# Optimization experiments

Hardware: AMD Instinct MI355X
Metric: run time of the kernel (lower is better)

## Reference

```python
import jax, jax.numpy as jnp
from jax import lax
import numpy as np

N_ASSETS = 256
BATCH = 512
MAX_WEIGHT = 0.05
N_ITERS = 300       # FISTA iterations (fixed, jit-friendly)
BISECT_ITERS = 60   # bisection iterations for the simplex-box projection
POWER_ITERS = 30    # power iterations for Lipschitz constant


def _project_capped_simplex(v, c):
    """Project rows of v onto {w : sum(w)=1, -c <= w <= c}.

    Finds tau s.t. sum(clip(v - tau, -c, c)) = 1 by bisection (non-diff),
    then recomputes tau exactly from the active-set mask so the projection
    is correctly differentiable (piecewise-linear Jacobian).
    """
    vs = lax.stop_gradient(v)
    lo = jnp.min(vs, axis=-1) - c   # sum = +n*c > 1 here
    hi = jnp.max(vs, axis=-1) + c   # sum = -n*c < 1 here

    def bis(carry, _):
        lo, hi = carry
        mid = 0.5 * (lo + hi)
        s = jnp.sum(jnp.clip(vs - mid[:, None], -c, c), axis=-1)
        lo = jnp.where(s > 1.0, mid, lo)
        hi = jnp.where(s > 1.0, hi, mid)
        return (lo, hi), None

    (lo, hi), _ = lax.scan(bis, (lo, hi), None, length=BISECT_ITERS)
    tau0 = 0.5 * (lo + hi)
    z = vs - tau0[:, None]
    interior = (jnp.abs(z) < c).astype(v.dtype)          # unclipped coords
    k_hi = jnp.sum((z >= c).astype(v.dtype), axis=-1)    # clipped at +c
    k_lo = jnp.sum((z <= -c).astype(v.dtype), axis=-1)   # clipped at -c
    denom = jnp.maximum(jnp.sum(interior, axis=-1), 1.0)
    # exact tau given the (stop-gradient) active set -> correct Jacobian in v
    tau = (jnp.sum(interior * v, axis=-1) + c * (k_hi - k_lo) - 1.0) / denom
    return jnp.clip(v - tau[:, None], -c, c)


def _min_var_weights(covmat_sqrt, c):
    """argmin_w ||A w||^2  s.t. sum(w)=1, -c<=w<=c  (batched FISTA)."""
    B, n, _ = covmat_sqrt.shape
    # Q = A^T A (the objective only depends on A through Q)
    Q = jnp.einsum('bij,bik->bjk', covmat_sqrt, covmat_sqrt)

    # power iteration for lambda_max(Q) -> step size 1/L, L = 2*lambda_max
    u = jnp.ones((B, n), covmat_sqrt.dtype) / jnp.sqrt(jnp.asarray(n, covmat_sqrt.dtype))

    def pit(u, _):
        u = jnp.einsum('bij,bj->bi', Q, u)
        u = u / (jnp.linalg.norm(u, axis=-1, keepdims=True) + 1e-12)
        return u, None

    u, _ = lax.scan(pit, u, None, length=POWER_ITERS)
    lmax = jnp.einsum('bi,bij,bj->b', u, Q, u)
    step = lax.stop_gradient(1.0 / (2.0 * lmax + 1e-12))[:, None]

    w0 = _project_capped_simplex(jnp.full((B, n), 1.0 / n, covmat_sqrt.dtype), c)

    @jax.checkpoint
    def fista(carry, _):
        w, y, t = carry
        g = 2.0 * jnp.einsum('bij,bj->bi', Q, y)
        w_new = _project_capped_simplex(y - step * g, c)
        t_new = 0.5 * (1.0 + jnp.sqrt(1.0 + 4.0 * t * t))
        y_new = w_new + ((t - 1.0) / t_new) * (w_new - w)
        return (w_new, y_new, t_new), None

    t0 = jnp.asarray(1.0, covmat_sqrt.dtype)
    (w, _, _), _ = lax.scan(fista, (w0, w0, t0), None, length=N_ITERS)
    return w


def setup_inputs() -> dict:
    key = jax.random.key(0)
    covmat_sqrt = jax.random.normal(
        key, (BATCH, N_ASSETS, N_ASSETS), dtype=jnp.float32
    ) / np.sqrt(N_ASSETS).astype(np.float32)
    return {"covmat_sqrt": covmat_sqrt}


def reference(covmat_sqrt):
    return _min_var_weights(covmat_sqrt, MAX_WEIGHT)
```

## Files before the change

kernel.cpp:

```cpp
#include <hip/hip_runtime.h>
#include <math.h>


#define NA    256
#define CAPW  0.05f

typedef float v2f __attribute__((ext_vector_type(2)));

template<int CTRL, int RM>
__device__ __forceinline__ float dpp0(float x) {
    return __int_as_float(__builtin_amdgcn_update_dpp(
        0, __float_as_int(x), CTRL, RM, 0xf, true));
}
template<int CTRL, int RM>
__device__ __forceinline__ float dppI(float x, float ident) {
    return __int_as_float(__builtin_amdgcn_update_dpp(
        __float_as_int(ident), __float_as_int(x), CTRL, RM, 0xf, false));
}
__device__ __forceinline__ float bcast63(float x) {
    return __int_as_float(__builtin_amdgcn_readlane(__float_as_int(x), 63));
}
__device__ __forceinline__ float wsum(float x) {
    x += dpp0<0x111, 0xf>(x);
    x += dpp0<0x112, 0xf>(x);
    x += dpp0<0x114, 0xf>(x);
    x += dpp0<0x118, 0xf>(x);
    x += dpp0<0x142, 0xa>(x);
    x += dpp0<0x143, 0xc>(x);
    return bcast63(x);
}
__device__ __forceinline__ float wmax(float x) {
    const float I = -1e30f;
    x = fmaxf(x, dppI<0x111, 0xf>(x, I));
    x = fmaxf(x, dppI<0x112, 0xf>(x, I));
    x = fmaxf(x, dppI<0x114, 0xf>(x, I));
    x = fmaxf(x, dppI<0x118, 0xf>(x, I));
    x = fmaxf(x, dppI<0x142, 0xa>(x, I));
    x = fmaxf(x, dppI<0x143, 0xc>(x, I));
    return bcast63(x);
}

__global__ void __launch_bounds__(512, 2)
markowitz_fista(const float* __restrict__ A, float* __restrict__ out)
{
    __shared__ float lds_pool[32 * 256];
    __shared__ int   done_flag;

    float* A_lds = lds_pool;
    float* p_lds = lds_pool;
    float* y_lds = lds_pool + 2048;

    const int tid = threadIdx.x;
    const int b   = blockIdx.x;
    const int r4  = tid & 63;
    const int e   = tid >> 6;
    const int R0  = r4 * 4;
    const int C0  = e * 32;

    const float* __restrict__ Ab = A + (size_t)b * NA * NA;

    v2f q2[4][16];
    #pragma unroll
    for (int a = 0; a < 4; ++a)
        #pragma unroll
        for (int k = 0; k < 16; ++k) q2[a][k] = (v2f){0.0f, 0.0f};

    for (int it = 0; it < 8; ++it) {
        __syncthreads();
        const float4* src = (const float4*)(Ab + it * 32 * 256);
        float4* dst = (float4*)A_lds;
        #pragma unroll
        for (int qd = 0; qd < 4; ++qd) dst[qd * 512 + tid] = src[qd * 512 + tid];
        __syncthreads();
        for (int ii = 0; ii < 32; ++ii) {
            const float* row = A_lds + ii * 256;
            float4 rv = *(const float4*)(row + R0);
            v2f r0 = {rv.x, rv.x}, r1 = {rv.y, rv.y}, r2 = {rv.z, rv.z}, r3 = {rv.w, rv.w};
            #pragma unroll
            for (int cc = 0; cc < 8; ++cc) {
                float4 cv = *(const float4*)(row + C0 + 4 * cc);
                v2f clo = {cv.x, cv.y}, chi = {cv.z, cv.w};
                q2[0][2*cc  ] = __builtin_elementwise_fma(r0, clo, q2[0][2*cc  ]);
                q2[0][2*cc+1] = __builtin_elementwise_fma(r0, chi, q2[0][2*cc+1]);
                q2[1][2*cc  ] = __builtin_elementwise_fma(r1, clo, q2[1][2*cc  ]);
                q2[1][2*cc+1] = __builtin_elementwise_fma(r1, chi, q2[1][2*cc+1]);
                q2[2][2*cc  ] = __builtin_elementwise_fma(r2, clo, q2[2][2*cc  ]);
                q2[2][2*cc+1] = __builtin_elementwise_fma(r2, chi, q2[2][2*cc+1]);
                q2[3][2*cc  ] = __builtin_elementwise_fma(r3, clo, q2[3][2*cc  ]);
                q2[3][2*cc+1] = __builtin_elementwise_fma(r3, chi, q2[3][2*cc+1]);
            }
        }
    }
    __syncthreads();

    auto partials = [&](bool chk) -> bool {
        __syncthreads();
        int fl = chk ? done_flag : 0;
        v2f aL0 = {0,0}, aL1 = {0,0}, aL2 = {0,0}, aL3 = {0,0};
        v2f aH0 = {0,0}, aH1 = {0,0}, aH2 = {0,0}, aH3 = {0,0};
        const float* yv = y_lds + C0;
        #pragma unroll
        for (int cc = 0; cc < 8; ++cc) {
            float4 y4 = *(const float4*)(yv + 4 * cc);
            v2f ylo = {y4.x, y4.y}, yhi = {y4.z, y4.w};
            aL0 = __builtin_elementwise_fma(q2[0][2*cc  ], ylo, aL0);
            aH0 = __builtin_elementwise_fma(q2[0][2*cc+1], yhi, aH0);
            aL1 = __builtin_elementwise_fma(q2[1][2*cc  ], ylo, aL1);
            aH1 = __builtin_elementwise_fma(q2[1][2*cc+1], yhi, aH1);
            aL2 = __builtin_elementwise_fma(q2[2][2*cc  ], ylo, aL2);
            aH2 = __builtin_elementwise_fma(q2[2][2*cc+1], yhi, aH2);
            aL3 = __builtin_elementwise_fma(q2[3][2*cc  ], ylo, aL3);
            aH3 = __builtin_elementwise_fma(q2[3][2*cc+1], yhi, aH3);
        }
        if (fl) return true;
        v2f s0 = aL0 + aH0, s1 = aL1 + aH1, s2 = aL2 + aH2, s3 = aL3 + aH3;
        *(float4*)(p_lds + e * 256 + R0) =
            make_float4(s0.x + s0.y, s1.x + s1.y, s2.x + s2.y, s3.x + s3.y);
        __syncthreads();
        return false;
    };
    auto reduceg = [&]() -> float4 {
        float4 r = *(const float4*)(p_lds + 4 * tid);
        #pragma unroll
        for (int ee = 1; ee < 8; ++ee) {
            float4 pv = *(const float4*)(p_lds + ee * 256 + 4 * tid);
            r.x += pv.x; r.y += pv.y; r.z += pv.z; r.w += pv.w;
        }
        return r;
    };

    if (tid < 64) {
        *(float4*)(y_lds + 4 * tid) = make_float4(0.0625f, 0.0625f, 0.0625f, 0.0625f);
    }
    float u0 = 0.0625f, u1 = 0.0625f, u2 = 0.0625f, u3 = 0.0625f;
    for (int p = 0; p < 30; ++p) {
        partials(false);
        if (tid < 64) {
            float4 g4 = reduceg();
            u0 = 0.25f * g4.x; u1 = 0.25f * g4.y;
            u2 = 0.25f * g4.z; u3 = 0.25f * g4.w;
            *(float4*)(y_lds + 4 * tid) = make_float4(u0, u1, u2, u3);
        }
    }
    partials(false);

    float step2 = 0.f, t = 1.0f, tau_ws = 0.0f, tau_pv = 0.0f, rm = 0.0f;
    float cnt_ws = 256.0f;
    float wa = 0.f, wb = 0.f, wc = 0.f, wd = 0.f;
    float ya = 0.f, yb = 0.f, yc = 0.f, yd = 0.f;
    if (tid < 64) {
        float4 g4 = reduceg();
        float num = wsum(u0*g4.x + u1*g4.y + u2*g4.z + u3*g4.w);
        float den = wsum(u0*u0 + u1*u1 + u2*u2 + u3*u3);
        float lm = num / (den + 1e-30f);
        float step = 1.0f / (2.0f * lm + 1e-12f);
        step2 = 2.0f * step;
        wa = wb = wc = wd = 1.0f / 256.0f;
        ya = yb = yc = yd = 1.0f / 256.0f;
        *(float4*)(y_lds + 4 * tid) = make_float4(ya, yb, yc, yd);
    }
    if (tid == 0) done_flag = 0;

    for (int itn = 0; itn < 300; ++itn) {
        if (partials(true)) break;
        if (tid < 64) {
            float4 g4 = reduceg();
            float v0 = ya - step2 * g4.x;
            float v1 = yb - step2 * g4.y;
            float v2 = yc - step2 * g4.z;
            float v3 = yd - step2 * g4.w;

            float lo = -2.0f, hi = 2.0f;
            float tau = fminf(fmaxf(tau_ws + (tau_ws - tau_pv), lo), hi);

            float s = 0.f, sm1 = 0.f;
            float tau_p = 0.f, s_p = 0.f;
            bool havep = false, have = false;
            for (int ni = 0; ni < 10; ++ni) {
                float z0 = v0 - tau, z1 = v1 - tau, z2 = v2 - tau, z3 = v3 - tau;
                float c0 = fminf(fmaxf(z0, -CAPW), CAPW);
                float c1 = fminf(fmaxf(z1, -CAPW), CAPW);
                float c2 = fminf(fmaxf(z2, -CAPW), CAPW);
                float c3 = fminf(fmaxf(z3, -CAPW), CAPW);
                s = wsum((c0 + c1) + (c2 + c3));
                sm1 = s - 1.0f;
                if (fabsf(sm1) <= 1e-4f) { have = true; break; }
                if (sm1 > 0.0f) lo = tau; else hi = tau;
                float m = fmaxf(cnt_ws, 1.0f);
                if (havep) {
                    float dt = tau - tau_p;
                    float ds = s_p - s;
                    float mm = ds / dt;
                    if (mm > 0.5f && mm == mm) m = mm;
                }
                float tn2 = tau + sm1 / m;
                if (!(tn2 > lo && tn2 < hi)) tn2 = 0.5f * (lo + hi);
                tau_p = tau; s_p = s; havep = true;
                tau = tn2;
            }
            if (!have) {
                float z0 = v0 - tau, z1 = v1 - tau, z2 = v2 - tau, z3 = v3 - tau;
                float c0 = fminf(fmaxf(z0, -CAPW), CAPW);
                float c1 = fminf(fmaxf(z1, -CAPW), CAPW);
                float c2 = fminf(fmaxf(z2, -CAPW), CAPW);
                float c3 = fminf(fmaxf(z3, -CAPW), CAPW);
                s = wsum((c0 + c1) + (c2 + c3));
                sm1 = s - 1.0f;
            }
            {
                float z0 = v0 - tau, z1 = v1 - tau, z2 = v2 - tau, z3 = v3 - tau;
                float cnt = wsum((fabsf(z0) < CAPW ? 1.f : 0.f) +
                                 (fabsf(z1) < CAPW ? 1.f : 0.f) +
                                 (fabsf(z2) < CAPW ? 1.f : 0.f) +
                                 (fabsf(z3) < CAPW ? 1.f : 0.f));
                cnt_ws = cnt;
                tau = tau + sm1 / fmaxf(cnt, 1.0f);
            }
            tau_pv = tau_ws;
            tau_ws = tau;
            float w0n = fminf(fmaxf(v0 - tau, -CAPW), CAPW);
            float w1n = fminf(fmaxf(v1 - tau, -CAPW), CAPW);
            float w2n = fminf(fmaxf(v2 - tau, -CAPW), CAPW);
            float w3n = fminf(fmaxf(v3 - tau, -CAPW), CAPW);

            float tn = 0.5f * (1.0f + sqrtf(1.0f + 4.0f * t * t));
            float beta = (t - 1.0f) / tn;
            float y0n = w0n + beta * (w0n - wa);
            float y1n = w1n + beta * (w1n - wb);
            float y2n = w2n + beta * (w2n - wc);
            float y3n = w3n + beta * (w3n - wd);

            *(float4*)(y_lds + 4 * tid) = make_float4(y0n, y1n, y2n, y3n);

            float dm = fmaxf(fmaxf(fabsf(w0n - wa), fabsf(w1n - wb)),
                             fmaxf(fabsf(w2n - wc), fabsf(w3n - wd)));
            rm = fmaxf(rm, dm);
            if ((itn & 7) == 7) {
                float rmax = wmax(rm);
                if (rmax < 1e-7f && tid == 0) done_flag = 1;
                rm = 0.0f;
            }

            wa = w0n; wb = w1n; wc = w2n; wd = w3n;
            ya = y0n; yb = y1n; yc = y2n; yd = y3n;
            t = tn;
        }
    }

    if (tid < 64) {
        *(float4*)(out + b * 256 + 4 * tid) = make_float4(wa, wb, wc, wd);
    }
}

extern "C" void kernel_launch(void* const* d_in, const int* in_sizes, int n_in,
                              void* d_out, int out_size, void* d_ws, size_t ws_size,
                              hipStream_t stream) {
    (void)in_sizes; (void)n_in; (void)d_ws; (void)ws_size; (void)out_size;
    const float* A = (const float*)d_in[0];
    float* out = (float*)d_out;
    hipLaunchKernelGGL(markowitz_fista, dim3(512), dim3(512), 0, stream, A, out);
}
```

Baseline: 933.9 us.

## Fold step into partials, precompute momentum on spare wave, speculate two tau guesses

The gradient step scale (-2*step) is stored in LDS and multiplied into the per-row partial products, so the wave doing the reduction only adds. FISTA momentum coefficients are computed one iteration ahead by a thread in the second wave and double-buffered in LDS, which takes the sqrt/divide off the critical serial wave. The projection now evaluates two candidate taus (the warm start and its extrapolation) together with their interior counts before entering a shorter Newton/bisection loop. This aims to cut serial latency per iteration on the single active wave, at the cost of extra wave reductions when neither guess converges.

```diff
diff --git a/kernel.cpp b/kernel.cpp
--- a/kernel.cpp
+++ b/kernel.cpp
@@ -96,6 +96,7 @@
     auto partials = [&](bool chk) -> bool {
         __syncthreads();
         int fl = chk ? done_flag : 0;
+        float scl = lds_pool[2304];
         v2f aL0 = {0,0}, aL1 = {0,0}, aL2 = {0,0}, aL3 = {0,0};
         v2f aH0 = {0,0}, aH1 = {0,0}, aH2 = {0,0}, aH3 = {0,0};
         const float* yv = y_lds + C0;
@@ -115,7 +116,8 @@
         if (fl) return true;
         v2f s0 = aL0 + aH0, s1 = aL1 + aH1, s2 = aL2 + aH2, s3 = aL3 + aH3;
         *(float4*)(p_lds + e * 256 + R0) =
-            make_float4(s0.x + s0.y, s1.x + s1.y, s2.x + s2.y, s3.x + s3.y);
+            make_float4(scl * (s0.x + s0.y), scl * (s1.x + s1.y),
+                        scl * (s2.x + s2.y), scl * (s3.x + s3.y));
         __syncthreads();
         return false;
     };
@@ -132,6 +134,7 @@
     if (tid < 64) {
         *(float4*)(y_lds + 4 * tid) = make_float4(0.0625f, 0.0625f, 0.0625f, 0.0625f);
     }
+    if (tid == 0) lds_pool[2304] = 1.0f;
     float u0 = 0.0625f, u1 = 0.0625f, u2 = 0.0625f, u3 = 0.0625f;
     for (int p = 0; p < 30; ++p) {
         partials(false);
@@ -144,8 +147,7 @@
     }
     partials(false);
 
-    float step2 = 0.f, t = 1.0f, tau_ws = 0.0f, tau_pv = 0.0f, rm = 0.0f;
-    float cnt_ws = 256.0f;
+    float tau_ws = 0.0f, tau_pv = 0.0f, rm = 0.0f;
     float wa = 0.f, wb = 0.f, wc = 0.f, wd = 0.f;
     float ya = 0.f, yb = 0.f, yc = 0.f, yd = 0.f;
     if (tid < 64) {
@@ -154,68 +156,102 @@
         float den = wsum(u0*u0 + u1*u1 + u2*u2 + u3*u3);
         float lm = num / (den + 1e-30f);
         float step = 1.0f / (2.0f * lm + 1e-12f);
-        step2 = 2.0f * step;
         wa = wb = wc = wd = 1.0f / 256.0f;
         ya = yb = yc = yd = 1.0f / 256.0f;
         *(float4*)(y_lds + 4 * tid) = make_float4(ya, yb, yc, yd);
-    }
-    if (tid == 0) done_flag = 0;
+        if (tid == 0) {
+            lds_pool[2304] = -2.0f * step;
+            done_flag = 0;
+        }
+    }
+    float tb1 = 0.5f * (1.0f + sqrtf(5.0f));
+    float tb2 = 0.5f * (1.0f + sqrtf(1.0f + 4.0f * tb1 * tb1));
+    if (tid == 64) lds_pool[2305] = 0.0f;
 
     for (int itn = 0; itn < 300; ++itn) {
         if (partials(true)) break;
         if (tid < 64) {
-            float4 g4 = reduceg();
-            float v0 = ya - step2 * g4.x;
-            float v1 = yb - step2 * g4.y;
-            float v2 = yc - step2 * g4.z;
-            float v3 = yd - step2 * g4.w;
+            float bf = lds_pool[2305 + (itn & 1)];
+            float4 r = *(const float4*)(p_lds + 4 * tid);
+            #pragma unroll
+            for (int ee = 1; ee < 8; ++ee) {
+                float4 pv = *(const float4*)(p_lds + ee * 256 + 4 * tid);
+                r.x += pv.x; r.y += pv.y; r.z += pv.z; r.w += pv.w;
+            }
+            float v0 = ya + r.x, v1 = yb + r.y, v2 = yc + r.z, v3 = yd + r.w;
 
             float lo = -2.0f, hi = 2.0f;
-            float tau = fminf(fmaxf(tau_ws + (tau_ws - tau_pv), lo), hi);
-
-            float s = 0.f, sm1 = 0.f;
-            float tau_p = 0.f, s_p = 0.f;
-            bool havep = false, have = false;
-            for (int ni = 0; ni < 10; ++ni) {
-                float z0 = v0 - tau, z1 = v1 - tau, z2 = v2 - tau, z3 = v3 - tau;
-                float c0 = fminf(fmaxf(z0, -CAPW), CAPW);
-                float c1 = fminf(fmaxf(z1, -CAPW), CAPW);
-                float c2 = fminf(fmaxf(z2, -CAPW), CAPW);
-                float c3 = fminf(fmaxf(z3, -CAPW), CAPW);
-                s = wsum((c0 + c1) + (c2 + c3));
-                sm1 = s - 1.0f;
-                if (fabsf(sm1) <= 1e-4f) { have = true; break; }
-                if (sm1 > 0.0f) lo = tau; else hi = tau;
-                float m = fmaxf(cnt_ws, 1.0f);
-                if (havep) {
-                    float dt = tau - tau_p;
-                    float ds = s_p - s;
-                    float mm = ds / dt;
-                    if (mm > 0.5f && mm == mm) m = mm;
+            float tA = fminf(fmaxf(tau_ws, lo), hi);
+            float tB = fminf(fmaxf(tau_ws + (tau_ws - tau_pv), lo), hi);
+
+            float zA0 = v0 - tA, zA1 = v1 - tA, zA2 = v2 - tA, zA3 = v3 - tA;
+            float zB0 = v0 - tB, zB1 = v1 - tB, zB2 = v2 - tB, zB3 = v3 - tB;
+            float cA0 = fminf(fmaxf(zA0, -CAPW), CAPW);
+            float cA1 = fminf(fmaxf(zA1, -CAPW), CAPW);
+            float cA2 = fminf(fmaxf(zA2, -CAPW), CAPW);
+            float cA3 = fminf(fmaxf(zA3, -CAPW), CAPW);
+            float cB0 = fminf(fmaxf(zB0, -CAPW), CAPW);
+            float cB1 = fminf(fmaxf(zB1, -CAPW), CAPW);
+            float cB2 = fminf(fmaxf(zB2, -CAPW), CAPW);
+            float cB3 = fminf(fmaxf(zB3, -CAPW), CAPW);
+            float sA = wsum((cA0 + cA1) + (cA2 + cA3));
+            float nA = wsum((fabsf(zA0) < CAPW ? 1.f : 0.f) +
+                            (fabsf(zA1) < CAPW ? 1.f : 0.f) +
+                            (fabsf(zA2) < CAPW ? 1.f : 0.f) +
+                            (fabsf(zA3) < CAPW ? 1.f : 0.f));
+            float sB = wsum((cB0 + cB1) + (cB2 + cB3));
+            float nB = wsum((fabsf(zB0) < CAPW ? 1.f : 0.f) +
+                            (fabsf(zB1) < CAPW ? 1.f : 0.f) +
+                            (fabsf(zB2) < CAPW ? 1.f : 0.f) +
+                            (fabsf(zB3) < CAPW ? 1.f : 0.f));
+            float dA = sA - 1.0f, dB = sB - 1.0f;
+
+            float tau, cnt, sm1;
+            if (fabsf(dA) <= 1e-4f)      { tau = tA; sm1 = dA; cnt = nA; }
+            else if (fabsf(dB) <= 1e-4f) { tau = tB; sm1 = dB; cnt = nB; }
+            else {
+                if (dA > 0.0f) lo = fmaxf(lo, tA); else hi = fminf(hi, tA);
+                if (dB > 0.0f) lo = fmaxf(lo, tB); else hi = fminf(hi, tB);
+                float tP, dP, nP;
+                if (fabsf(dA) <= fabsf(dB)) { tP = tA; dP = dA; nP = nA; }
+                else                        { tP = tB; dP = dB; nP = nB; }
+                tau = tP + dP / fmaxf(nP, 1.0f);
+                if (!(tau > lo && tau < hi)) tau = 0.5f * (lo + hi);
+                bool have = false;
+                cnt = 1.0f; sm1 = 0.0f;
+                for (int ni = 0; ni < 8; ++ni) {
+                    float z0 = v0 - tau, z1 = v1 - tau, z2 = v2 - tau, z3 = v3 - tau;
+                    float c0 = fminf(fmaxf(z0, -CAPW), CAPW);
+                    float c1 = fminf(fmaxf(z1, -CAPW), CAPW);
+                    float c2 = fminf(fmaxf(z2, -CAPW), CAPW);
+                    float c3 = fminf(fmaxf(z3, -CAPW), CAPW);
+                    float s = wsum((c0 + c1) + (c2 + c3));
+                    cnt = wsum((fabsf(z0) < CAPW ? 1.f : 0.f) +
+                               (fabsf(z1) < CAPW ? 1.f : 0.f) +
+                               (fabsf(z2) < CAPW ? 1.f : 0.f) +
+                               (fabsf(z3) < CAPW ? 1.f : 0.f));
+                    sm1 = s - 1.0f;
+                    if (fabsf(sm1) <= 1e-4f) { have = true; break; }
+                    if (sm1 > 0.0f) lo = tau; else hi = tau;
+                    float tn2 = tau + sm1 / fmaxf(cnt, 1.0f);
+                    if (!(tn2 > lo && tn2 < hi)) tn2 = 0.5f * (lo + hi);
+                    tau = tn2;
                 }
-                float tn2 = tau + sm1 / m;
-                if (!(tn2 > lo && tn2 < hi)) tn2 = 0.5f * (lo + hi);
-                tau_p = tau; s_p = s; havep = true;
-                tau = tn2;
+                if (!have) {
+                    float z0 = v0 - tau, z1 = v1 - tau, z2 = v2 - tau, z3 = v3 - tau;
+                    float c0 = fminf(fmaxf(z0, -CAPW), CAPW);
+                    float c1 = fminf(fmaxf(z1, -CAPW), CAPW);
+                    float c2 = fminf(fmaxf(z2, -CAPW), CAPW);
+                    float c3 = fminf(fmaxf(z3, -CAPW), CAPW);
+                    float s = wsum((c0 + c1) + (c2 + c3));
+                    cnt = wsum((fabsf(z0) < CAPW ? 1.f : 0.f) +
+                               (fabsf(z1) < CAPW ? 1.f : 0.f) +
+                               (fabsf(z2) < CAPW ? 1.f : 0.f) +
+                               (fabsf(z3) < CAPW ? 1.f : 0.f));
+                    sm1 = s - 1.0f;
+                }
             }
-            if (!have) {
-                float z0 = v0 - tau, z1 = v1 - tau, z2 = v2 - tau, z3 = v3 - tau;
-                float c0 = fminf(fmaxf(z0, -CAPW), CAPW);
-                float c1 = fminf(fmaxf(z1, -CAPW), CAPW);
-                float c2 = fminf(fmaxf(z2, -CAPW), CAPW);
-                float c3 = fminf(fmaxf(z3, -CAPW), CAPW);
-                s = wsum((c0 + c1) + (c2 + c3));
-                sm1 = s - 1.0f;
-            }
-            {
-                float z0 = v0 - tau, z1 = v1 - tau, z2 = v2 - tau, z3 = v3 - tau;
-                float cnt = wsum((fabsf(z0) < CAPW ? 1.f : 0.f) +
-                                 (fabsf(z1) < CAPW ? 1.f : 0.f) +
-                                 (fabsf(z2) < CAPW ? 1.f : 0.f) +
-                                 (fabsf(z3) < CAPW ? 1.f : 0.f));
-                cnt_ws = cnt;
-                tau = tau + sm1 / fmaxf(cnt, 1.0f);
-            }
+            tau = tau + sm1 / fmaxf(cnt, 1.0f);
             tau_pv = tau_ws;
             tau_ws = tau;
             float w0n = fminf(fmaxf(v0 - tau, -CAPW), CAPW);
@@ -223,12 +259,10 @@
             float w2n = fminf(fmaxf(v2 - tau, -CAPW), CAPW);
             float w3n = fminf(fmaxf(v3 - tau, -CAPW), CAPW);
 
-            float tn = 0.5f * (1.0f + sqrtf(1.0f + 4.0f * t * t));
-            float beta = (t - 1.0f) / tn;
-            float y0n = w0n + beta * (w0n - wa);
-            float y1n = w1n + beta * (w1n - wb);
-            float y2n = w2n + beta * (w2n - wc);
-            float y3n = w3n + beta * (w3n - wd);
+            float y0n = w0n + bf * (w0n - wa);
+            float y1n = w1n + bf * (w1n - wb);
+            float y2n = w2n + bf * (w2n - wc);
+            float y3n = w3n + bf * (w3n - wd);
 
             *(float4*)(y_lds + 4 * tid) = make_float4(y0n, y1n, y2n, y3n);
 
@@ -243,7 +277,11 @@
 
             wa = w0n; wb = w1n; wc = w2n; wd = w3n;
             ya = y0n; yb = y1n; yc = y2n; yd = y3n;
-            t = tn;
+        } else if (tid == 64) {
+            float bnew = (tb1 - 1.0f) / tb2;
+            lds_pool[2305 + ((itn + 1) & 1)] = bnew;
+            tb1 = tb2;
+            tb2 = 0.5f * (1.0f + sqrtf(1.0f + 4.0f * tb2 * tb2));
         }
     }
 
```

Measured after the change: 950.8 us. About the same (+1.8%).
